# Performance work log

Measured on AMD Instinct MI355X. Metric: run time of the kernel, lower is better.

Reference implementation:

```python
import jax, jax.numpy as jnp
import numpy as np

N = 256          # batch size
C = 100          # nb_classes
D = 512          # sz_embed
SCALE = 3.0
EPS = 1e-12      # F.normalize eps
M = N * (N - 1) // 2  # number of (i<j) candidate pairs


def l2norm(x):
    # matches F.normalize(p=2, dim=-1) with eps=1e-12
    return x / jnp.maximum(jnp.linalg.norm(x, axis=-1, keepdims=True), EPS)


def dist_block(A, B):
    # squared euclidean distance block of pairwise_distance(cat([A,B]))[0][:len(A), len(A):]
    # (off-diagonal block, so the eye-masking in the original is a no-op; negatives zeroed)
    d = (A * A).sum(-1, keepdims=True) + (B * B).sum(-1)[None, :] - 2.0 * (A @ B.T)
    return jnp.maximum(d, 0.0)


def setup_inputs() -> dict:
    key = jax.random.key(0)
    k1, k2, k3 = jax.random.split(key, 3)
    X = jax.random.normal(k1, (N, D), dtype=jnp.float32)
    proxies = jax.random.normal(k2, (C, D), dtype=jnp.float32) / 8.0
    T = jax.random.randint(k3, (N,), 0, C)
    indices = jnp.arange(N)  # unused by forward, kept for signature fidelity
    return {"X": X, "proxies": proxies, "T": T, "indices": indices}


def reference(X, proxies, T, indices):
    Pn = SCALE * l2norm(proxies)           # (C, D)
    Xn = SCALE * l2norm(X)                 # (N, D)
    IP = Xn @ Pn.T                         # (N, C) inner-product block

    # --- intercls_mixup (method=1, uncertainty-guided lambdas) ---
    # all i<j pairs; same-class pairs are masked out (original skips them in a Python loop)
    i1, i2 = jnp.triu_indices(N, k=1)      # (M,), (M,)
    diff = T[i1] != T[i2]                  # (M,) valid cross-class pairs
    c1, c2 = T[i1], T[i2]

    X1P1 = jnp.clip(IP[i1, c1], -1.0, 1.0)
    X1P2 = jnp.clip(IP[i1, c2], -1.0, 1.0)
    X2P1 = jnp.clip(IP[i2, c1], -1.0, 1.0)
    X2P2 = jnp.clip(IP[i2, c2], -1.0, 1.0)
    lam = jnp.clip((X2P2 - X2P1) / (X2P2 - X2P1 + X1P1 - X1P2), 0.3, 0.7)
    lam = jnp.where(diff, lam, 0.5)        # neutralize masked (same-class) pairs

    virt = lam[:, None] * Xn[i1] + (1.0 - lam[:, None]) * Xn[i2]  # (M, D)
    virt = l2norm(virt)

    # --- proxy-NCA loss over real + virtual samples ---
    Xall = jnp.concatenate([Xn, SCALE * virt], axis=0)            # (N+M, D)
    Dall = dist_block(Xall, Pn)                                   # (N+M, C)
    logsm = jax.nn.log_softmax(-Dall, axis=-1)

    loss_real = -logsm[jnp.arange(N), T]                          # one-hot targets
    lv = logsm[N:]                                                # (M, C)
    rows = jnp.arange(M)
    # virtual soft targets: lam*onehot(c1) + (1-lam)*onehot(c2)
    loss_virt = -(lam * lv[rows, c1] + (1.0 - lam) * lv[rows, c2])

    total = loss_real.sum() + jnp.sum(jnp.where(diff, loss_virt, 0.0))
    count = N + diff.sum()
    return total / count
```

## Files before the change

kernel.cpp:

```cpp
#include <hip/hip_runtime.h>
#include <hip/hip_bf16.h>
#include <math.h>

#define N_ 256
#define C_ 100
#define D_ 512
#define LOG2E 1.44269504088896f

#define WS_GX  0
#define WS_GTP 65536
#define WS_RN  91136

typedef __attribute__((ext_vector_type(8))) short short8;
typedef __attribute__((ext_vector_type(4))) float floatx4;

__device__ inline float waveReduceSum(float v) {
    #pragma unroll
    for (int off = 32; off > 0; off >>= 1) v += __shfl_xor(v, off, 64);
    return v;
}
__device__ inline float clip1(float x) { return fminf(fmaxf(x, -1.0f), 1.0f); }

__device__ inline short8 cvt8(float4 a, float4 b) {
    union { __hip_bfloat16 h[8]; short8 s; } u;
    u.h[0] = __float2bfloat16(a.x); u.h[1] = __float2bfloat16(a.y);
    u.h[2] = __float2bfloat16(a.z); u.h[3] = __float2bfloat16(a.w);
    u.h[4] = __float2bfloat16(b.x); u.h[5] = __float2bfloat16(b.y);
    u.h[6] = __float2bfloat16(b.z); u.h[7] = __float2bfloat16(b.w);
    return u.s;
}

__global__ __launch_bounds__(256)
void gemm_kernel(const float* __restrict__ X, const float* __restrict__ P,
                 float* __restrict__ ws) {
    float* Gx  = ws + WS_GX;
    float* GTP = ws + WS_GTP;
    float* rn  = ws + WS_RN;
    __shared__ floatx4 accl[3][64];
    int tile = blockIdx.x;
    int t = threadIdx.x, w = t >> 6, lane = t & 63;
    int r = lane & 15, quad = lane >> 4;
    const float *arow, *brow;
    int tm, tn, mode;
    if (tile < 256) {
        mode = 0; tm = tile >> 4; tn = tile & 15;
        arow = X + (size_t)(tm * 16 + r) * D_;
        brow = X + (size_t)(tn * 16 + r) * D_;
    } else if (tile < 368) {
        int u = tile - 256; mode = 1; tm = u / 7; tn = u - tm * 7;
        int pb = tn * 16 + r; if (pb >= C_) pb = 0;
        arow = X + (size_t)(tm * 16 + r) * D_;
        brow = P + (size_t)pb * D_;
    } else {
        mode = 2; tm = tile - 368; tn = tm;
        int pa = tm * 16 + r; if (pa >= C_) pa = 0;
        arow = P + (size_t)pa * D_;
        brow = arow;
    }
    floatx4 acc = {0.0f, 0.0f, 0.0f, 0.0f};
    int k0 = w * 128;
    #pragma unroll
    for (int kk = 0; kk < 128; kk += 32) {
        const float4* ap = (const float4*)(arow + k0 + kk + quad * 8);
        const float4* bp = (const float4*)(brow + k0 + kk + quad * 8);
        short8 av = cvt8(ap[0], ap[1]);
        short8 bv = cvt8(bp[0], bp[1]);
        acc = __builtin_amdgcn_mfma_f32_16x16x32_bf16(av, bv, acc, 0, 0, 0);
    }
    if (w) accl[w - 1][lane] = acc;
    __syncthreads();
    if (w == 0) {
        acc += accl[0][lane]; acc += accl[1][lane]; acc += accl[2][lane];
        if (mode == 0) {
            int row0 = tm * 16 + quad * 4, col = tn * 16 + r;
            #pragma unroll
            for (int i = 0; i < 4; ++i) Gx[(row0 + i) * 256 + col] = acc[i];
            if (tm == tn && (r >> 2) == quad)
                rn[tm * 16 + r] = 3.0f * rsqrtf(fmaxf(acc[r & 3], 1e-24f));
        } else if (mode == 1) {
            int c = tn * 16 + r;
            if (c < C_) {
                int row0 = tm * 16 + quad * 4;
                #pragma unroll
                for (int i = 0; i < 4; ++i)
                    GTP[(c >> 2) * 1024 + (row0 + i) * 4 + (c & 3)] = acc[i];
            }
        } else {
            if ((r >> 2) == quad) {
                int pr = tm * 16 + r;
                if (pr < C_) rn[256 + pr] = 3.0f * rsqrtf(fmaxf(acc[r & 3], 1e-24f));
            }
        }
    }
}

__global__ __launch_bounds__(1024)
void pair_kernel(const float* __restrict__ ws, const int* __restrict__ T,
                 float* __restrict__ out) {
    const float* Gx  = ws + WS_GX;
    const float4* G4 = (const float4*)(ws + WS_GTP);
    const float* rn  = ws + WS_RN;
    __shared__ int Tl[256];
    __shared__ int hist[C_];
    __shared__ float sxl[256];
    __shared__ float red[16];

    int t = threadIdx.x, w = t >> 6, lane = t & 63;
    int b = blockIdx.x;
    if (t < 256) { Tl[t] = T[t]; sxl[t] = rn[t]; }
    if (t < C_) hist[t] = 0;
    __syncthreads();
    if (t < 256) atomicAdd(&hist[Tl[t]], 1);

    int m = t >> 2, p = t & 3;
    int t1 = Tl[b];
    float s1 = sxl[b];
    bool diag = (m == b);
    bool act = diag || ((m > b) && (Tl[m] != t1));
    float contrib = 0.0f;
    if (__ballot(act)) {
        if (act) {
            int t2 = Tl[m];
            float sc2 = sxl[m];
            float sp1 = rn[256 + t1], sp2 = rn[256 + t2];
            const float* GTPf = (const float*)G4;
            float ip11 = GTPf[(t1 >> 2) * 1024 + b * 4 + (t1 & 3)] * s1 * sp1;
            float ip12 = GTPf[(t2 >> 2) * 1024 + b * 4 + (t2 & 3)] * s1 * sp2;
            float ip21 = GTPf[(t1 >> 2) * 1024 + m * 4 + (t1 & 3)] * sc2 * sp1;
            float ip22 = GTPf[(t2 >> 2) * 1024 + m * 4 + (t2 & 3)] * sc2 * sp2;
            float X1P1 = clip1(ip11), X1P2 = clip1(ip12);
            float X2P1 = clip1(ip21), X2P2 = clip1(ip22);
            float num = X2P2 - X2P1;
            float den = num + X1P1 - X1P2;
            float lam = fminf(fmaxf(num / den, 0.3f), 0.7f);
            if (diag) lam = 1.0f;
            float oml = 1.0f - lam;
            float g = Gx[b * 256 + m] * s1 * sc2;
            float wn2 = 9.0f * (lam * lam + oml * oml) + 2.0f * lam * oml * g;
            float ss2 = 6.0f * rsqrtf(fmaxf(wn2, 1e-24f));
            float la = ss2 * lam * s1 * LOG2E, lb = ss2 * oml * sc2 * LOG2E;
            float sm = 0.0f;
            #pragma unroll
            for (int k = 0; k < 7; ++k) {
                int q = p + 4 * k;
                if (q < 25) {
                    float4 a1 = G4[q * 256 + b];
                    float4 a2 = G4[q * 256 + m];
                    const float4 s4 = *(const float4*)(rn + 256 + q * 4);
                    sm += exp2f(s4.x * (la * a1.x + lb * a2.x));
                    sm += exp2f(s4.y * (la * a1.y + lb * a2.y));
                    sm += exp2f(s4.z * (la * a1.z + lb * a2.z));
                    sm += exp2f(s4.w * (la * a1.w + lb * a2.w));
                }
            }
            sm += __shfl_xor(sm, 1, 64);
            sm += __shfl_xor(sm, 2, 64);
            if (p == 0) {
                float LSE = logf(sm);
                float ec1 = ss2 * (lam * ip11 + oml * ip21);
                float ec2 = ss2 * (lam * ip12 + oml * ip22);
                contrib = LSE - lam * ec1 - oml * ec2;
            }
        }
    }
    float rsum = waveReduceSum(contrib);
    if (lane == 0) red[w] = rsum;
    __syncthreads();
    if (w == 0) {
        float same;
        { float n = (float)hist[lane]; same = 0.5f * n * (n - 1.0f); }
        if (lane + 64 < C_) { float n = (float)hist[lane + 64]; same += 0.5f * n * (n - 1.0f); }
        float bs = (lane < 16) ? red[lane] : 0.0f;
        same = waveReduceSum(same);
        bs = waveReduceSum(bs);
        if (lane == 0) atomicAdd(out, bs / (32896.0f - same));
    }
}

extern "C" void kernel_launch(void* const* d_in, const int* in_sizes, int n_in,
                              void* d_out, int out_size, void* d_ws, size_t ws_size,
                              hipStream_t stream) {
    const float* X = (const float*)d_in[0];
    const float* P = (const float*)d_in[1];
    const int*   T = (const int*)d_in[2];
    float* ws = (float*)d_ws;
    float* out = (float*)d_out;

    gemm_kernel<<<375, 256, 0, stream>>>(X, P, ws);
    pair_kernel<<<N_, 1024, 0, stream>>>(ws, T, out);
}
```

Measured before the change: 71.52 us.

## Compute only upper-triangle Gram tiles and stage per-row proxy data in shared memory

The gemm kernel now computes only the upper-triangular 16x16 tiles of X·Xᵀ (136 instead of 256), which cuts the grid from 375 to 255 blocks. The pair kernel only reads Gx for m>=b, so the skipped lower tiles are never needed. In the pair kernel, each wave stages the row-b inner products and proxy scales in LDS, and each thread preloads its row-m values into registers before the active branch. The histogram atomics move after the main compute, which removes the initial barrier so global loads can issue early. The cost is extra registers for the seven float4 preloads, redundant per-wave LDS copies, and a serial loop for tile index decoding.

After: 69.44 us (median of 2 runs). 2.9% less time.

```diff
diff --git a/kernel.cpp b/kernel.cpp
--- a/kernel.cpp
+++ b/kernel.cpp
@@ -42,17 +42,20 @@
     int r = lane & 15, quad = lane >> 4;
     const float *arow, *brow;
     int tm, tn, mode;
-    if (tile < 256) {
-        mode = 0; tm = tile >> 4; tn = tile & 15;
+    if (tile < 136) {
+        mode = 0;
+        int u = tile; tm = 0;
+        while (u >= 16 - tm) { u -= 16 - tm; ++tm; }
+        tn = tm + u;
         arow = X + (size_t)(tm * 16 + r) * D_;
         brow = X + (size_t)(tn * 16 + r) * D_;
-    } else if (tile < 368) {
-        int u = tile - 256; mode = 1; tm = u / 7; tn = u - tm * 7;
+    } else if (tile < 248) {
+        int u = tile - 136; mode = 1; tm = u / 7; tn = u - tm * 7;
         int pb = tn * 16 + r; if (pb >= C_) pb = 0;
         arow = X + (size_t)(tm * 16 + r) * D_;
         brow = P + (size_t)pb * D_;
     } else {
-        mode = 2; tm = tile - 368; tn = tm;
+        mode = 2; tm = tile - 248; tn = tm;
         int pa = tm * 16 + r; if (pa >= C_) pa = 0;
         arow = P + (size_t)pa * D_;
         brow = arow;
@@ -97,74 +100,88 @@
 __global__ __launch_bounds__(1024)
 void pair_kernel(const float* __restrict__ ws, const int* __restrict__ T,
                  float* __restrict__ out) {
-    const float* Gx  = ws + WS_GX;
-    const float4* G4 = (const float4*)(ws + WS_GTP);
-    const float* rn  = ws + WS_RN;
-    __shared__ int Tl[256];
+    const float* Gx   = ws + WS_GX;
+    const float4* G4  = (const float4*)(ws + WS_GTP);
+    const float* GTPf = ws + WS_GTP;
+    const float* rn   = ws + WS_RN;
+    __shared__ __attribute__((aligned(16))) float wbufA[16][104];
+    __shared__ __attribute__((aligned(16))) float wbufS[16][104];
     __shared__ int hist[C_];
-    __shared__ float sxl[256];
     __shared__ float red[16];
 
     int t = threadIdx.x, w = t >> 6, lane = t & 63;
     int b = blockIdx.x;
-    if (t < 256) { Tl[t] = T[t]; sxl[t] = rn[t]; }
+    int m = t >> 2, p = t & 3;
+
+    int t1 = T[b];
+    int t2 = T[m];
+    float s1 = rn[b], sc2 = rn[m];
+    float graw = 0.0f;
+    if (m >= b) graw = Gx[b * 256 + m];
+    float4 a2r[7];
+    #pragma unroll
+    for (int k = 0; k < 7; ++k) {
+        int q = p + 4 * k;
+        a2r[k] = (float4){0.f, 0.f, 0.f, 0.f};
+        if (q < 25 && m >= b) a2r[k] = G4[q * 256 + m];
+    }
+    int Tt = (t < 256) ? T[t] : 0;
     if (t < C_) hist[t] = 0;
-    __syncthreads();
-    if (t < 256) atomicAdd(&hist[Tl[t]], 1);
-
-    int m = t >> 2, p = t & 3;
-    int t1 = Tl[b];
-    float s1 = sxl[b];
+    if (lane < 25) {
+        float4 av = G4[lane * 256 + b];
+        float4 sv = *(const float4*)(rn + 256 + lane * 4);
+        *(float4*)&wbufA[w][lane * 4] = av;
+        *(float4*)&wbufS[w][lane * 4] = sv;
+    }
+
     bool diag = (m == b);
-    bool act = diag || ((m > b) && (Tl[m] != t1));
+    bool act = diag || ((m > b) && (t2 != t1));
     float contrib = 0.0f;
-    if (__ballot(act)) {
-        if (act) {
-            int t2 = Tl[m];
-            float sc2 = sxl[m];
-            float sp1 = rn[256 + t1], sp2 = rn[256 + t2];
-            const float* GTPf = (const float*)G4;
-            float ip11 = GTPf[(t1 >> 2) * 1024 + b * 4 + (t1 & 3)] * s1 * sp1;
-            float ip12 = GTPf[(t2 >> 2) * 1024 + b * 4 + (t2 & 3)] * s1 * sp2;
-            float ip21 = GTPf[(t1 >> 2) * 1024 + m * 4 + (t1 & 3)] * sc2 * sp1;
-            float ip22 = GTPf[(t2 >> 2) * 1024 + m * 4 + (t2 & 3)] * sc2 * sp2;
-            float X1P1 = clip1(ip11), X1P2 = clip1(ip12);
-            float X2P1 = clip1(ip21), X2P2 = clip1(ip22);
-            float num = X2P2 - X2P1;
-            float den = num + X1P1 - X1P2;
-            float lam = fminf(fmaxf(num / den, 0.3f), 0.7f);
-            if (diag) lam = 1.0f;
-            float oml = 1.0f - lam;
-            float g = Gx[b * 256 + m] * s1 * sc2;
-            float wn2 = 9.0f * (lam * lam + oml * oml) + 2.0f * lam * oml * g;
-            float ss2 = 6.0f * rsqrtf(fmaxf(wn2, 1e-24f));
-            float la = ss2 * lam * s1 * LOG2E, lb = ss2 * oml * sc2 * LOG2E;
-            float sm = 0.0f;
-            #pragma unroll
-            for (int k = 0; k < 7; ++k) {
-                int q = p + 4 * k;
-                if (q < 25) {
-                    float4 a1 = G4[q * 256 + b];
-                    float4 a2 = G4[q * 256 + m];
-                    const float4 s4 = *(const float4*)(rn + 256 + q * 4);
-                    sm += exp2f(s4.x * (la * a1.x + lb * a2.x));
-                    sm += exp2f(s4.y * (la * a1.y + lb * a2.y));
-                    sm += exp2f(s4.z * (la * a1.z + lb * a2.z));
-                    sm += exp2f(s4.w * (la * a1.w + lb * a2.w));
-                }
-            }
-            sm += __shfl_xor(sm, 1, 64);
-            sm += __shfl_xor(sm, 2, 64);
-            if (p == 0) {
-                float LSE = logf(sm);
-                float ec1 = ss2 * (lam * ip11 + oml * ip21);
-                float ec2 = ss2 * (lam * ip12 + oml * ip22);
-                contrib = LSE - lam * ec1 - oml * ec2;
+    if (act) {
+        float ip11r = wbufA[w][t1], ip12r = wbufA[w][t2];
+        float sp1 = wbufS[w][t1], sp2 = wbufS[w][t2];
+        float ip21r = GTPf[(t1 >> 2) * 1024 + m * 4 + (t1 & 3)];
+        float ip22r = GTPf[(t2 >> 2) * 1024 + m * 4 + (t2 & 3)];
+        float ip11 = ip11r * s1 * sp1, ip12 = ip12r * s1 * sp2;
+        float ip21 = ip21r * sc2 * sp1, ip22 = ip22r * sc2 * sp2;
+        float X1P1 = clip1(ip11), X1P2 = clip1(ip12);
+        float X2P1 = clip1(ip21), X2P2 = clip1(ip22);
+        float num = X2P2 - X2P1;
+        float den = num + X1P1 - X1P2;
+        float lam = fminf(fmaxf(num / den, 0.3f), 0.7f);
+        if (diag) lam = 1.0f;
+        float oml = 1.0f - lam;
+        float g = graw * s1 * sc2;
+        float wn2 = 9.0f * (lam * lam + oml * oml) + 2.0f * lam * oml * g;
+        float ss2 = 6.0f * rsqrtf(fmaxf(wn2, 1e-24f));
+        float la = ss2 * lam * s1 * LOG2E, lb = ss2 * oml * sc2 * LOG2E;
+        float sm = 0.0f;
+        #pragma unroll
+        for (int k = 0; k < 7; ++k) {
+            int q = p + 4 * k;
+            if (q < 25) {
+                float4 a1 = *(const float4*)&wbufA[w][q * 4];
+                float4 s4 = *(const float4*)&wbufS[w][q * 4];
+                float4 a2 = a2r[k];
+                sm += exp2f(s4.x * (la * a1.x + lb * a2.x));
+                sm += exp2f(s4.y * (la * a1.y + lb * a2.y));
+                sm += exp2f(s4.z * (la * a1.z + lb * a2.z));
+                sm += exp2f(s4.w * (la * a1.w + lb * a2.w));
             }
         }
+        sm += __shfl_xor(sm, 1, 64);
+        sm += __shfl_xor(sm, 2, 64);
+        if (p == 0) {
+            float LSE = logf(sm);
+            float ec1 = ss2 * (lam * ip11 + oml * ip21);
+            float ec2 = ss2 * (lam * ip12 + oml * ip22);
+            contrib = LSE - lam * ec1 - oml * ec2;
+        }
     }
     float rsum = waveReduceSum(contrib);
     if (lane == 0) red[w] = rsum;
+    __syncthreads();
+    if (t < 256) atomicAdd(&hist[Tt], 1);
     __syncthreads();
     if (w == 0) {
         float same;
@@ -186,6 +203,6 @@
     float* ws = (float*)d_ws;
     float* out = (float*)d_out;
 
-    gemm_kernel<<<375, 256, 0, stream>>>(X, P, ws);
+    gemm_kernel<<<255, 256, 0, stream>>>(X, P, ws);
     pair_kernel<<<N_, 1024, 0, stream>>>(ws, T, out);
 }
```
